# Performance work log

Hardware: AMD Instinct MI355X
Metric: run time of the kernel (lower is better)

Reference implementation:

```python
import jax, jax.numpy as jnp
import numpy as np

RX = 2  # matches init rx
RY = 2  # matches init ry


def _bilinear_gather(img, coords):
    """Bilinear sample with zero padding (mirrors grid_sample align_corners=True, padding_mode='zeros').
    img: [C,H,W]; coords: [P,2] pixel-space (x,y). Returns [C,P]."""
    C, H, W = img.shape
    x, y = coords[:, 0], coords[:, 1]
    x0, y0 = jnp.floor(x), jnp.floor(y)
    wx, wy = x - x0, y - y0

    def tap(xi, yi, w):
        valid = (xi >= 0) & (xi <= W - 1) & (yi >= 0) & (yi <= H - 1)
        xc = jnp.clip(xi, 0, W - 1).astype(jnp.int32)
        yc = jnp.clip(yi, 0, H - 1).astype(jnp.int32)
        v = img[:, yc, xc]  # [C,P] gather
        return v * (w * valid.astype(w.dtype))[None, :]

    return (tap(x0, y0, (1 - wx) * (1 - wy)) + tap(x0 + 1, y0, wx * (1 - wy))
            + tap(x0, y0 + 1, (1 - wx) * wy) + tap(x0 + 1, y0 + 1, wx * wy))


def _local_cost_volume(flow, f1, f2, rx, ry):
    """build_sample_cv: windowed bilinear gather of f2 around (grid + flow), dot with f1.
    Returns cv [N,H,W,2ry+1,2rx+1] with window ordered (dy,dx)."""
    N, C, H, W = f1.shape
    dt = f1.dtype
    gy, gx = jnp.meshgrid(jnp.arange(H, dtype=dt), jnp.arange(W, dtype=dt), indexing='ij')
    base = jnp.stack([gx, gy], 0)[None]            # [1,2,H,W] (x,y) like coords_grid
    cen = (base + flow).transpose(0, 2, 3, 1)       # [N,H,W,2]
    dx = jnp.linspace(-rx, rx, 2 * rx + 1).astype(dt)
    dy = jnp.linspace(-ry, ry, 2 * ry + 1).astype(dt)
    mgy, mgx = jnp.meshgrid(dy, dx, indexing='ij')  # [dH,dW]
    off = jnp.stack([mgx, mgy], -1)                 # [dH,dW,2] (x,y)
    dH, dW = 2 * ry + 1, 2 * rx + 1
    coords = cen[:, None, None] + off[None, :, :, None, None, :]  # [N,dH,dW,H,W,2]
    coords = coords.reshape(N, dH * dW * H * W, 2)
    samp = jax.vmap(_bilinear_gather)(f2, coords)   # [N,C,dH*dW*H*W]
    samp = samp.reshape(N, C, dH, dW, H, W)
    # cv[n,h,w,i,j] = sum_c f1[n,c,h,w] * f2_sampled[n,c,i,j,h,w]
    cv = jnp.einsum('nchw,ncijhw->nhwij', f1, samp)
    return cv


def setup_inputs() -> dict:
    key = jax.random.key(0)
    k1, k2, k3 = jax.random.split(key, 3)
    N, C, H, W = 2, 256, 55, 128
    return {
        'flow': jax.random.normal(k1, (N, 2, H, W), dtype=jnp.float32),
        'f1': jax.random.normal(k2, (N, C, H, W), dtype=jnp.float32),
        'f2': jax.random.normal(k3, (N, C, H, W), dtype=jnp.float32),
    }


def reference(flow, f1, f2):
    cv = _local_cost_volume(flow, f1, f2, RX, RY)   # [N,H,W,dH,dW]
    N, H, W, dH, dW = cv.shape
    flat = cv.reshape(N, H, W, dH * dW)
    # WTA over the last two (window) dims, as in get_argmax_NHW_xy_last_th
    wta_val = jnp.max(flat, axis=-1)
    idx = jnp.argmax(flat, axis=-1)
    wta_xy = jnp.stack([idx % dW, idx // dW], axis=0)  # [2,N,H,W] (x,y)
    return cv, wta_val, wta_xy
```

## Files before the change

### kernel.cpp

```cpp
#include <hip/hip_runtime.h>

#define N_   2
#define C_   256
#define H_   55
#define W_   128
#define HW_  (H_ * W_)
#define NPIX (N_ * HW_)
#define PB   16
#define PW   4
#define NBLK (NPIX / PB)
#define BPX  (NBLK / 8)
#define F1LD 260

#define OFF_CV  0
#define OFF_VAL (NPIX * 25)
#define OFF_XY  (OFF_VAL + NPIX)

typedef float f32x4 __attribute__((ext_vector_type(4)));

__global__ __launch_bounds__(256) void transpose_f2(const float* __restrict__ f2,
                                                    float* __restrict__ f2t) {
    __shared__ float tile[64][65];
    const int n = blockIdx.z;
    const float* __restrict__ src = f2 + (size_t)n * C_ * HW_;
    float* __restrict__ dst = f2t + (size_t)n * HW_ * C_;

    const int p0 = blockIdx.x * 64;
    const int c0 = blockIdx.y * 64;
    const int q = threadIdx.x & 15;
    const int r = threadIdx.x >> 4;

    #pragma unroll
    for (int rr = r; rr < 64; rr += 16) {
        const f32x4 v = __builtin_nontemporal_load(
            (const f32x4*)(src + (size_t)(c0 + rr) * HW_ + p0 + q * 4));
        tile[rr][q * 4 + 0] = v.x;
        tile[rr][q * 4 + 1] = v.y;
        tile[rr][q * 4 + 2] = v.z;
        tile[rr][q * 4 + 3] = v.w;
    }
    __syncthreads();

    #pragma unroll
    for (int j = 0; j < 4; ++j) {
        const int pr = r + 16 * j;
        float4 v;
        v.x = tile[q * 4 + 0][pr];
        v.y = tile[q * 4 + 1][pr];
        v.z = tile[q * 4 + 2][pr];
        v.w = tile[q * 4 + 3][pr];
        *(float4*)(dst + (size_t)(p0 + pr) * C_ + c0 + q * 4) = v;
    }
}

__device__ __forceinline__ float dot4(const float4 a, const float4 b) {
    return a.x * b.x + a.y * b.y + a.z * b.z + a.w * b.w;
}

__device__ __forceinline__ float dpp_add16(float x) {
    int v;
    v = __builtin_amdgcn_update_dpp(0, __float_as_int(x), 0xB1, 0xF, 0xF, true);
    x += __int_as_float(v);
    v = __builtin_amdgcn_update_dpp(0, __float_as_int(x), 0x4E, 0xF, 0xF, true);
    x += __int_as_float(v);
    v = __builtin_amdgcn_update_dpp(0, __float_as_int(x), 0x141, 0xF, 0xF, true);
    x += __int_as_float(v);
    v = __builtin_amdgcn_update_dpp(0, __float_as_int(x), 0x140, 0xF, 0xF, true);
    x += __int_as_float(v);
    return x;
}

__global__ __launch_bounds__(256) void costvol_kernel(const float* __restrict__ flow,
                                                      const float* __restrict__ f1,
                                                      const float* __restrict__ f2t,
                                                      float* __restrict__ out) {
    __shared__ float f1sh[PB][F1LD];
    __shared__ float Dsh[4][36];

    const int b    = blockIdx.x;
    const int xcd  = b & 7;
    const int kk   = b >> 3;
    const int pix0 = (xcd * BPX + kk) * PB;
    const int n     = pix0 / HW_;
    const int prem0 = pix0 - n * HW_;
    const int h     = prem0 >> 7;
    const int w0    = prem0 & (W_ - 1);

    {
        const int px4   = threadIdx.x & 3;
        const int cbase = threadIdx.x >> 2;
        #pragma unroll
        for (int it = 0; it < 4; ++it) {
            const int c = cbase + it * 64;
            const f32x4 v = __builtin_nontemporal_load(
                (const f32x4*)(f1 + ((size_t)n * C_ + c) * HW_ + prem0 + px4 * 4));
            f1sh[px4 * 4 + 0][c] = v.x;
            f1sh[px4 * 4 + 1][c] = v.y;
            f1sh[px4 * 4 + 2][c] = v.z;
            f1sh[px4 * 4 + 3][c] = v.w;
        }
    }
    __syncthreads();

    const int wv   = threadIdx.x >> 6;
    const int lane = threadIdx.x & 63;
    const int sgrp = lane >> 4;
    const int cgrp = lane & 15;

    const int s0 = sgrp,      s1 = 4 + sgrp,  s2 = 8 + sgrp,  s3 = 12 + sgrp;
    const int s4 = 16 + sgrp, s5 = 20 + sgrp, s6 = 24 + sgrp, s7 = 28 + sgrp;
    const int s8 = 32 + sgrp;
    const int ly0 = s0 / 6, lx0 = s0 - 6 * ly0;
    const int ly1 = s1 / 6, lx1 = s1 - 6 * ly1;
    const int ly2 = s2 / 6, lx2 = s2 - 6 * ly2;
    const int ly3 = s3 / 6, lx3 = s3 - 6 * ly3;
    const int ly4 = s4 / 6, lx4 = s4 - 6 * ly4;
    const int ly5 = s5 / 6, lx5 = s5 - 6 * ly5;
    const int ly6 = s6 / 6, lx6 = s6 - 6 * ly6;
    const int ly7 = s7 / 6, lx7 = s7 - 6 * ly7;
    const int ly8 = s8 / 6, lx8 = s8 - 6 * ly8;

    const float4* __restrict__ f2base = (const float4*)(f2t + (size_t)n * HW_ * C_);
    const float* __restrict__ flown   = flow + (size_t)n * 2 * HW_;

    for (int pp = 0; pp < PW; ++pp) {
        const int pl  = wv * PW + pp;
        const int pix = pix0 + pl;
        const int w   = w0 + pl;

        const float fx = __builtin_nontemporal_load(flown + h * W_ + w);
        const float fy = __builtin_nontemporal_load(flown + HW_ + h * W_ + w);
        const float cx = (float)w + fx;
        const float cy = (float)h + fy;
        const float x0f = floorf(cx), y0f = floorf(cy);
        const float wx = cx - x0f, wy = cy - y0f;
        const int ix0 = (int)x0f, iy0 = (int)y0f;

        const float* fr = &f1sh[pl][cgrp * 4];
        const float4 a0 = *(const float4*)(fr);
        const float4 a1 = *(const float4*)(fr + 64);
        const float4 a2 = *(const float4*)(fr + 128);
        const float4 a3 = *(const float4*)(fr + 192);

        float4 A0, A1, A2, A3, B0, B1, B2, B3, C0, C1, C2, C3;

#define BPTR(LY, LX)                                                            \
    (f2base + (size_t)(min(max(iy0 - 2 + (LY), 0), H_ - 1) * W_ +               \
                       min(max(ix0 - 2 + (LX), 0), W_ - 1)) * (C_ / 4) + cgrp)
#define LDX(R0, R1, R2, R3, LY, LX) {                                           \
        const float4* __restrict__ bp = BPTR(LY, LX);                           \
        R0 = bp[0]; R1 = bp[16]; R2 = bp[32]; R3 = bp[48]; }
#define CMP(R0, R1, R2, R3, LY, LX)                                             \
    ((((unsigned)(iy0 - 2 + (LY)) < (unsigned)H_) &&                            \
      ((unsigned)(ix0 - 2 + (LX)) < (unsigned)W_))                              \
         ? (dot4(a0, R0) + dot4(a1, R1) + dot4(a2, R2) + dot4(a3, R3)) : 0.f)

        LDX(A0, A1, A2, A3, ly0, lx0)
        LDX(B0, B1, B2, B3, ly1, lx1)
        LDX(C0, C1, C2, C3, ly2, lx2)
        const float D0 = CMP(A0, A1, A2, A3, ly0, lx0); LDX(A0, A1, A2, A3, ly3, lx3)
        const float D1 = CMP(B0, B1, B2, B3, ly1, lx1); LDX(B0, B1, B2, B3, ly4, lx4)
        const float D2 = CMP(C0, C1, C2, C3, ly2, lx2); LDX(C0, C1, C2, C3, ly5, lx5)
        const float D3 = CMP(A0, A1, A2, A3, ly3, lx3); LDX(A0, A1, A2, A3, ly6, lx6)
        const float D4 = CMP(B0, B1, B2, B3, ly4, lx4); LDX(B0, B1, B2, B3, ly7, lx7)
        const float D5 = CMP(C0, C1, C2, C3, ly5, lx5); LDX(C0, C1, C2, C3, ly8, lx8)
        const float D6 = CMP(A0, A1, A2, A3, ly6, lx6);
        const float D7 = CMP(B0, B1, B2, B3, ly7, lx7);
        const float D8 = CMP(C0, C1, C2, C3, ly8, lx8);
#undef BPTR
#undef LDX
#undef CMP

        float t;
        t = dpp_add16(D0); if (cgrp == 0) Dsh[wv][0 * 4 + sgrp] = t;
        t = dpp_add16(D1); if (cgrp == 0) Dsh[wv][1 * 4 + sgrp] = t;
        t = dpp_add16(D2); if (cgrp == 0) Dsh[wv][2 * 4 + sgrp] = t;
        t = dpp_add16(D3); if (cgrp == 0) Dsh[wv][3 * 4 + sgrp] = t;
        t = dpp_add16(D4); if (cgrp == 0) Dsh[wv][4 * 4 + sgrp] = t;
        t = dpp_add16(D5); if (cgrp == 0) Dsh[wv][5 * 4 + sgrp] = t;
        t = dpp_add16(D6); if (cgrp == 0) Dsh[wv][6 * 4 + sgrp] = t;
        t = dpp_add16(D7); if (cgrp == 0) Dsh[wv][7 * 4 + sgrp] = t;
        t = dpp_add16(D8); if (cgrp == 0) Dsh[wv][8 * 4 + sgrp] = t;
        __builtin_amdgcn_wave_barrier();

        float cv = 0.f;
        if (lane < 25) {
            const int i = lane / 5, j = lane - i * 5;
            const float D00 = Dsh[wv][i * 6 + j];
            const float D01 = Dsh[wv][i * 6 + j + 1];
            const float D10 = Dsh[wv][i * 6 + j + 6];
            const float D11 = Dsh[wv][i * 6 + j + 7];
            cv = (1.f - wx) * (1.f - wy) * D00 + wx * (1.f - wy) * D01
               + (1.f - wx) * wy * D10 + wx * wy * D11;
            __builtin_nontemporal_store(cv, out + OFF_CV + (size_t)pix * 25 + lane);
        }

        float v  = (lane < 25) ? cv : -3.4e38f;
        int  idx = (lane < 25) ? lane : 25;
        #pragma unroll
        for (int off = 16; off >= 1; off >>= 1) {
            const float v2 = __shfl_down(v, off, 32);
            const int   i2 = __shfl_down(idx, off, 32);
            if (v2 > v || (v2 == v && i2 < idx)) { v = v2; idx = i2; }
        }
        if (lane == 0) {
            __builtin_nontemporal_store(v, out + OFF_VAL + pix);
            __builtin_nontemporal_store((float)(idx % 5), out + OFF_XY + pix);
            __builtin_nontemporal_store((float)(idx / 5), out + OFF_XY + NPIX + pix);
        }
        __builtin_amdgcn_wave_barrier();
    }
}

extern "C" void kernel_launch(void* const* d_in, const int* in_sizes, int n_in,
                              void* d_out, int out_size, void* d_ws, size_t ws_size,
                              hipStream_t stream) {
    const float* flow = (const float*)d_in[0];
    const float* f1   = (const float*)d_in[1];
    const float* f2   = (const float*)d_in[2];
    float* out = (float*)d_out;

    float* f2t = (float*)d_ws;

    transpose_f2<<<dim3(HW_ / 64, C_ / 64, N_), 256, 0, stream>>>(f2, f2t);
    costvol_kernel<<<dim3(NBLK), 256, 0, stream>>>(flow, f1, f2t, out);
}
```

Baseline: 105.1 us.

## Stage f2 window taps into LDS via global_load_lds with double buffering

Shrinks the block from 16 to 4 pixels so each wave handles a single pixel, and precomputes flow-derived coordinates and weights in shared memory. The f2 taps of the 6x6 window are now fetched straight into LDS with global_load_lds into two alternating stage buffers, with explicit vmcnt waits so the next set of loads is in flight while the current one is reduced. The goal is to cut register pressure and overlap load latency with compute, and the smaller blocks give more of them in flight. The cost is four times as many blocks, extra LDS traffic, and correctness that depends on the hand-counted vmcnt waits.

```diff
diff --git a/kernel.cpp b/kernel.cpp
--- a/kernel.cpp
+++ b/kernel.cpp
@@ -6,11 +6,9 @@
 #define W_   128
 #define HW_  (H_ * W_)
 #define NPIX (N_ * HW_)
-#define PB   16
-#define PW   4
+#define PB   4
 #define NBLK (NPIX / PB)
 #define BPX  (NBLK / 8)
-#define F1LD 260
 
 #define OFF_CV  0
 #define OFF_VAL (NPIX * 25)
@@ -70,13 +68,46 @@
     return x;
 }
 
+__device__ __forceinline__ void blend_wta(const float* __restrict__ Drow,
+                                          float wx, float wy, int pix, int lane,
+                                          float* __restrict__ out) {
+    float cv = 0.f;
+    if (lane < 25) {
+        const int i = lane / 5, j = lane - i * 5;
+        const float D00 = Drow[i * 6 + j];
+        const float D01 = Drow[i * 6 + j + 1];
+        const float D10 = Drow[i * 6 + j + 6];
+        const float D11 = Drow[i * 6 + j + 7];
+        cv = (1.f - wx) * (1.f - wy) * D00 + wx * (1.f - wy) * D01
+           + (1.f - wx) * wy * D10 + wx * wy * D11;
+        __builtin_nontemporal_store(cv, out + OFF_CV + (size_t)pix * 25 + lane);
+    }
+    float v  = (lane < 25) ? cv : -3.4e38f;
+    int  idx = (lane < 25) ? lane : 25;
+    #pragma unroll
+    for (int off = 16; off >= 1; off >>= 1) {
+        const float v2 = __shfl_down(v, off, 32);
+        const int   i2 = __shfl_down(idx, off, 32);
+        if (v2 > v || (v2 == v && i2 < idx)) { v = v2; idx = i2; }
+    }
+    if (lane == 0) {
+        __builtin_nontemporal_store(v, out + OFF_VAL + pix);
+        __builtin_nontemporal_store((float)(idx % 5), out + OFF_XY + pix);
+        __builtin_nontemporal_store((float)(idx / 5), out + OFF_XY + NPIX + pix);
+    }
+}
+
 __global__ __launch_bounds__(256) void costvol_kernel(const float* __restrict__ flow,
                                                       const float* __restrict__ f1,
                                                       const float* __restrict__ f2t,
                                                       float* __restrict__ out) {
-    __shared__ float f1sh[PB][F1LD];
+    __shared__ float f1sh[PB][C_];
+    __shared__ __align__(16) float stage[4][2][4][C_];
     __shared__ float Dsh[4][36];
-
+    __shared__ float wxs[PB], wys[PB];
+    __shared__ int   ix0s[PB], iy0s[PB];
+
+    const int tid  = threadIdx.x;
     const int b    = blockIdx.x;
     const int xcd  = b & 7;
     const int kk   = b >> 3;
@@ -86,26 +117,34 @@
     const int h     = prem0 >> 7;
     const int w0    = prem0 & (W_ - 1);
 
+    const float* __restrict__ flown = flow + (size_t)n * 2 * HW_;
+    if (tid < PB) {
+        const float fx = flown[h * W_ + w0 + tid];
+        const float fy = flown[HW_ + h * W_ + w0 + tid];
+        const float cx = (float)(w0 + tid) + fx;
+        const float cy = (float)h + fy;
+        const float x0f = floorf(cx), y0f = floorf(cy);
+        wxs[tid] = cx - x0f;  wys[tid] = cy - y0f;
+        ix0s[tid] = (int)x0f; iy0s[tid] = (int)y0f;
+    }
+
     {
-        const int px4   = threadIdx.x & 3;
-        const int cbase = threadIdx.x >> 2;
-        #pragma unroll
-        for (int it = 0; it < 4; ++it) {
-            const int c = cbase + it * 64;
-            const f32x4 v = __builtin_nontemporal_load(
-                (const f32x4*)(f1 + ((size_t)n * C_ + c) * HW_ + prem0 + px4 * 4));
-            f1sh[px4 * 4 + 0][c] = v.x;
-            f1sh[px4 * 4 + 1][c] = v.y;
-            f1sh[px4 * 4 + 2][c] = v.z;
-            f1sh[px4 * 4 + 3][c] = v.w;
-        }
+        const f32x4 v = __builtin_nontemporal_load(
+            (const f32x4*)(f1 + ((size_t)n * C_ + tid) * HW_ + prem0));
+        f1sh[0][tid] = v.x;
+        f1sh[1][tid] = v.y;
+        f1sh[2][tid] = v.z;
+        f1sh[3][tid] = v.w;
     }
     __syncthreads();
 
-    const int wv   = threadIdx.x >> 6;
-    const int lane = threadIdx.x & 63;
+    const int wv   = tid >> 6;
+    const int lane = tid & 63;
     const int sgrp = lane >> 4;
     const int cgrp = lane & 15;
+
+    const int   ix0 = ix0s[wv], iy0 = iy0s[wv];
+    const float wx  = wxs[wv],  wy  = wys[wv];
 
     const int s0 = sgrp,      s1 = 4 + sgrp,  s2 = 8 + sgrp,  s3 = 12 + sgrp;
     const int s4 = 16 + sgrp, s5 = 20 + sgrp, s6 = 24 + sgrp, s7 = 28 + sgrp;
@@ -120,96 +159,57 @@
     const int ly7 = s7 / 6, lx7 = s7 - 6 * ly7;
     const int ly8 = s8 / 6, lx8 = s8 - 6 * ly8;
 
-    const float4* __restrict__ f2base = (const float4*)(f2t + (size_t)n * HW_ * C_);
-    const float* __restrict__ flown   = flow + (size_t)n * 2 * HW_;
-
-    for (int pp = 0; pp < PW; ++pp) {
-        const int pl  = wv * PW + pp;
-        const int pix = pix0 + pl;
-        const int w   = w0 + pl;
-
-        const float fx = __builtin_nontemporal_load(flown + h * W_ + w);
-        const float fy = __builtin_nontemporal_load(flown + HW_ + h * W_ + w);
-        const float cx = (float)w + fx;
-        const float cy = (float)h + fy;
-        const float x0f = floorf(cx), y0f = floorf(cy);
-        const float wx = cx - x0f, wy = cy - y0f;
-        const int ix0 = (int)x0f, iy0 = (int)y0f;
-
-        const float* fr = &f1sh[pl][cgrp * 4];
-        const float4 a0 = *(const float4*)(fr);
-        const float4 a1 = *(const float4*)(fr + 64);
-        const float4 a2 = *(const float4*)(fr + 128);
-        const float4 a3 = *(const float4*)(fr + 192);
-
-        float4 A0, A1, A2, A3, B0, B1, B2, B3, C0, C1, C2, C3;
-
-#define BPTR(LY, LX)                                                            \
-    (f2base + (size_t)(min(max(iy0 - 2 + (LY), 0), H_ - 1) * W_ +               \
-                       min(max(ix0 - 2 + (LX), 0), W_ - 1)) * (C_ / 4) + cgrp)
-#define LDX(R0, R1, R2, R3, LY, LX) {                                           \
-        const float4* __restrict__ bp = BPTR(LY, LX);                           \
-        R0 = bp[0]; R1 = bp[16]; R2 = bp[32]; R3 = bp[48]; }
-#define CMP(R0, R1, R2, R3, LY, LX)                                             \
-    ((((unsigned)(iy0 - 2 + (LY)) < (unsigned)H_) &&                            \
-      ((unsigned)(ix0 - 2 + (LX)) < (unsigned)W_))                              \
-         ? (dot4(a0, R0) + dot4(a1, R1) + dot4(a2, R2) + dot4(a3, R3)) : 0.f)
-
-        LDX(A0, A1, A2, A3, ly0, lx0)
-        LDX(B0, B1, B2, B3, ly1, lx1)
-        LDX(C0, C1, C2, C3, ly2, lx2)
-        const float D0 = CMP(A0, A1, A2, A3, ly0, lx0); LDX(A0, A1, A2, A3, ly3, lx3)
-        const float D1 = CMP(B0, B1, B2, B3, ly1, lx1); LDX(B0, B1, B2, B3, ly4, lx4)
-        const float D2 = CMP(C0, C1, C2, C3, ly2, lx2); LDX(C0, C1, C2, C3, ly5, lx5)
-        const float D3 = CMP(A0, A1, A2, A3, ly3, lx3); LDX(A0, A1, A2, A3, ly6, lx6)
-        const float D4 = CMP(B0, B1, B2, B3, ly4, lx4); LDX(B0, B1, B2, B3, ly7, lx7)
-        const float D5 = CMP(C0, C1, C2, C3, ly5, lx5); LDX(C0, C1, C2, C3, ly8, lx8)
-        const float D6 = CMP(A0, A1, A2, A3, ly6, lx6);
-        const float D7 = CMP(B0, B1, B2, B3, ly7, lx7);
-        const float D8 = CMP(C0, C1, C2, C3, ly8, lx8);
-#undef BPTR
-#undef LDX
-#undef CMP
-
-        float t;
-        t = dpp_add16(D0); if (cgrp == 0) Dsh[wv][0 * 4 + sgrp] = t;
-        t = dpp_add16(D1); if (cgrp == 0) Dsh[wv][1 * 4 + sgrp] = t;
-        t = dpp_add16(D2); if (cgrp == 0) Dsh[wv][2 * 4 + sgrp] = t;
-        t = dpp_add16(D3); if (cgrp == 0) Dsh[wv][3 * 4 + sgrp] = t;
-        t = dpp_add16(D4); if (cgrp == 0) Dsh[wv][4 * 4 + sgrp] = t;
-        t = dpp_add16(D5); if (cgrp == 0) Dsh[wv][5 * 4 + sgrp] = t;
-        t = dpp_add16(D6); if (cgrp == 0) Dsh[wv][6 * 4 + sgrp] = t;
-        t = dpp_add16(D7); if (cgrp == 0) Dsh[wv][7 * 4 + sgrp] = t;
-        t = dpp_add16(D8); if (cgrp == 0) Dsh[wv][8 * 4 + sgrp] = t;
-        __builtin_amdgcn_wave_barrier();
-
-        float cv = 0.f;
-        if (lane < 25) {
-            const int i = lane / 5, j = lane - i * 5;
-            const float D00 = Dsh[wv][i * 6 + j];
-            const float D01 = Dsh[wv][i * 6 + j + 1];
-            const float D10 = Dsh[wv][i * 6 + j + 6];
-            const float D11 = Dsh[wv][i * 6 + j + 7];
-            cv = (1.f - wx) * (1.f - wy) * D00 + wx * (1.f - wy) * D01
-               + (1.f - wx) * wy * D10 + wx * wy * D11;
-            __builtin_nontemporal_store(cv, out + OFF_CV + (size_t)pix * 25 + lane);
-        }
-
-        float v  = (lane < 25) ? cv : -3.4e38f;
-        int  idx = (lane < 25) ? lane : 25;
-        #pragma unroll
-        for (int off = 16; off >= 1; off >>= 1) {
-            const float v2 = __shfl_down(v, off, 32);
-            const int   i2 = __shfl_down(idx, off, 32);
-            if (v2 > v || (v2 == v && i2 < idx)) { v = v2; idx = i2; }
-        }
-        if (lane == 0) {
-            __builtin_nontemporal_store(v, out + OFF_VAL + pix);
-            __builtin_nontemporal_store((float)(idx % 5), out + OFF_XY + pix);
-            __builtin_nontemporal_store((float)(idx / 5), out + OFF_XY + NPIX + pix);
-        }
-        __builtin_amdgcn_wave_barrier();
-    }
+    const float* __restrict__ f2n = f2t + (size_t)n * HW_ * C_;
+    const float* fr = &f1sh[wv][cgrp * 4];
+    const float4 a0 = *(const float4*)(fr);
+    const float4 a1 = *(const float4*)(fr + 64);
+    const float4 a2 = *(const float4*)(fr + 128);
+    const float4 a3 = *(const float4*)(fr + 192);
+
+#define ISS1(P, Q, BUF) {                                                        \
+        constexpr int s_  = 4 * (P) + (Q);                                       \
+        constexpr int dy_ = s_ / 6;                                              \
+        constexpr int dx_ = s_ - 6 * dy_;                                        \
+        const int scy = min(max(iy0 - 2 + dy_, 0), H_ - 1);                      \
+        const int scx = min(max(ix0 - 2 + dx_, 0), W_ - 1);                      \
+        const float* gsrc = f2n + ((size_t)(scy * W_ + scx) << 8) + (lane << 2); \
+        __builtin_amdgcn_global_load_lds(                                        \
+            (const __attribute__((address_space(1))) void*)gsrc,                 \
+            (__attribute__((address_space(3))) void*)&stage[wv][BUF][Q][0],      \
+            16, 0, 0); }
+#define ISSUE(P, BUF) ISS1(P, 0, BUF) ISS1(P, 1, BUF) ISS1(P, 2, BUF) ISS1(P, 3, BUF)
+
+#define VMW(NN) { asm volatile("s_waitcnt vmcnt(" #NN ")" ::: "memory");         \
+                  __builtin_amdgcn_sched_barrier(0); }
+
+#define COMPUTE(P, BUF) {                                                        \
+        const int sy = iy0 - 2 + ly##P, sx = ix0 - 2 + lx##P;                    \
+        const float msk = (((unsigned)sy < (unsigned)H_) &&                      \
+                          ((unsigned)sx < (unsigned)W_)) ? 1.f : 0.f;            \
+        const float4* bp = (const float4*)&stage[wv][BUF][sgrp][0] + cgrp;       \
+        const float part = msk * (dot4(a0, bp[0])  + dot4(a1, bp[16])            \
+                                + dot4(a2, bp[32]) + dot4(a3, bp[48]));          \
+        const float t_ = dpp_add16(part);                                        \
+        if (cgrp == 0) Dsh[wv][4 * (P) + sgrp] = t_; }
+
+    ISSUE(0, 0)
+    ISSUE(1, 1) VMW(4) COMPUTE(0, 0)
+    ISSUE(2, 0) VMW(4) COMPUTE(1, 1)
+    ISSUE(3, 1) VMW(4) COMPUTE(2, 0)
+    ISSUE(4, 0) VMW(4) COMPUTE(3, 1)
+    ISSUE(5, 1) VMW(4) COMPUTE(4, 0)
+    ISSUE(6, 0) VMW(4) COMPUTE(5, 1)
+    ISSUE(7, 1) VMW(4) COMPUTE(6, 0)
+    ISSUE(8, 0) VMW(4) COMPUTE(7, 1)
+    VMW(0)      COMPUTE(8, 0)
+
+#undef ISS1
+#undef ISSUE
+#undef VMW
+#undef COMPUTE
+
+    __builtin_amdgcn_wave_barrier();
+    blend_wta(Dsh[wv], wx, wy, pix0 + wv, lane, out);
 }
 
 extern "C" void kernel_launch(void* const* d_in, const int* in_sizes, int n_in,
```

Measured after the change: 113.2 us. +7.7%, slower.
